# Kernel tuning notes

Measured on AMD Instinct MI355X. Metric: run time of the kernel, lower is better.

The kernel has to match this reference:

```python
import jax, jax.numpy as jnp
import numpy as np
from jax import lax

# db6 filters (pywt convention). rec_lo are the standard Daubechies-12 scaling coefs.
REC_LO = np.array([0.11154074335008017, 0.4946238903983854, 0.7511339080215775,
                   0.3152503517092432, -0.22626469396516913, -0.12976686756709563,
                   0.09750160558707936, 0.02752286553001629, -0.031582039318031156,
                   0.0005538422009938016, 0.004777257511010651, -0.00107730108499558])
L = 12
# qmf: rec_hi[n] = (-1)^n * rec_lo[L-1-n]
REC_HI = np.array([(-1.0)**n * REC_LO[L - 1 - n] for n in range(L)])
DEC_LO = REC_LO[::-1].copy()
DEC_HI = REC_HI[::-1].copy()
J = 8  # level1
DN = ('NCH', 'OIH', 'NCH')

def _afb(x):
    # one analysis level, symmetric padding (matches pytorch_wavelets afb1d).
    B, C, N = x.shape
    outsize = (N + L - 1) // 2
    p = 2 * (outsize - 1) - N + L
    xp = jnp.pad(x, ((0, 0), (0, 0), (p // 2, p - p // 2)), mode='symmetric')
    # torch conv1d correlates with reversed dec filters == rec filters
    k = jnp.stack([jnp.asarray(REC_LO, x.dtype), jnp.asarray(REC_HI, x.dtype)])[:, None, :]
    y = lax.conv_general_dilated(xp.reshape(B * C, 1, -1), k, (2,), 'VALID',
                                 dimension_numbers=DN)  # (B*C, 2, outsize)
    y = y.reshape(B, C, 2, outsize)
    return y[:, :, 0], y[:, :, 1]

def _sfb(lo, hi):
    # one synthesis level: conv_transpose1d(stride=2, padding=L-2) with rec filters
    # == dilate-by-2, pad 1 each side, correlate with flipped rec (= dec) filters.
    B, C, N = lo.shape
    def up(z, k):
        kk = jnp.asarray(k, z.dtype)[None, None, :]
        return lax.conv_general_dilated(z.reshape(B * C, 1, N), kk, (1,), [(1, 1)],
                                        lhs_dilation=(2,), dimension_numbers=DN).reshape(B, C, -1)
    return up(lo, DEC_LO) + up(hi, DEC_HI)  # length 2N - L + 2

def setup_inputs() -> dict:
    key = jax.random.key(0)
    k1, k2, k3 = jax.random.split(key, 3)
    Cin, Cout = 64, 64
    scale = 1.0 / (Cin * Cout)
    x = jax.random.normal(k1, (256, Cin, 1024), dtype=jnp.float32)
    weights1 = scale * jax.random.uniform(k2, (Cin, Cout, J + 6), dtype=jnp.float32)
    weights2 = scale * jax.random.uniform(k3, (Cin, Cout, J + 6), dtype=jnp.float32)
    return {'x': x, 'weights1': weights1, 'weights2': weights2}

def reference(x, weights1, weights2):
    # DWT decompose: yh[0] finest ... yh[-1] coarsest (pytorch_wavelets order)
    lo = x
    highs = []
    for _ in range(J):
        lo, hi = _afb(lo)
        highs.append(hi)
    # channel mix on coarsest approx and coarsest detail
    lo = jnp.einsum('bix,iox->box', lo, weights1)
    highs[-1] = jnp.einsum('bix,iox->box', highs[-1], weights2)
    # IDWT reconstruct, trimming odd-length mismatches like pytorch_wavelets
    y = lo
    for hi in highs[::-1]:
        if y.shape[-1] > hi.shape[-1]:
            y = y[..., :hi.shape[-1]]
        y = _sfb(y, hi)
    return y
```

## Files before the change

### kernel.cpp

```cpp
#include <hip/hip_runtime.h>

typedef float f2 __attribute__((ext_vector_type(2)));
typedef _Float16 half_t;
typedef _Float16 h4 __attribute__((ext_vector_type(4)));
typedef _Float16 h8 __attribute__((ext_vector_type(8)));

static constexpr float REC_LO[12] = {
  0.11154074335008017f, 0.4946238903983854f, 0.7511339080215775f, 0.3152503517092432f,
  -0.22626469396516913f, -0.12976686756709563f, 0.09750160558707936f, 0.02752286553001629f,
  -0.031582039318031156f, 0.0005538422009938016f, 0.004777257511010651f, -0.00107730108499558f };
static constexpr float REC_HI[12] = {
  -0.00107730108499558f, -0.004777257511010651f, 0.0005538422009938016f, 0.031582039318031156f,
  0.02752286553001629f, -0.09750160558707936f, -0.12976686756709563f, 0.22626469396516913f,
  0.3152503517092432f, -0.7511339080215775f, 0.4946238903983854f, -0.11154074335008017f };
static constexpr float DEC_LO[12] = {
  -0.00107730108499558f, 0.004777257511010651f, 0.0005538422009938016f, -0.031582039318031156f,
  0.02752286553001629f, 0.09750160558707936f, -0.12976686756709563f, -0.22626469396516913f,
  0.3152503517092432f, 0.7511339080215775f, 0.4946238903983854f, 0.11154074335008017f };
static constexpr float DEC_HI[12] = {
  -0.11154074335008017f, 0.4946238903983854f, -0.7511339080215775f, 0.3152503517092432f,
  0.22626469396516913f, -0.12976686756709563f, -0.09750160558707936f, 0.02752286553001629f,
  0.031582039318031156f, 0.0005538422009938016f, -0.004777257511010651f, -0.00107730108499558f };

#define NROWS 16384
#define WPB 4


__global__ __launch_bounds__(256) void afb_fused(const float* __restrict__ x,
                                                 half_t* __restrict__ ws) {
  __shared__ float sA[WPB][548];
  __shared__ float sB[WPB][296];
  constexpr int LENS[9] = {1024, 517, 264, 137, 74, 42, 26, 18, 14};
  constexpr int HSTR[8] = {520, 264, 144, 80, 48, 32, 24, 16};
  constexpr int HOFF[8] = {0, 520, 784, 928, 1008, 1056, 1088, 1112};
  const int wid = threadIdx.x >> 6;
  const int lane = threadIdx.x & 63;
  const int row = blockIdx.x * WPB + wid;
  float* bufA = sA[wid];
  float* bufB = sB[wid];
  const float* xrow = x + (size_t)row * 1024;
  half_t* hi0 = ws + (size_t)row * 520;

  {
    const int q = lane;
    const int base = (q == 0) ? 0 : 16 * q - 12;
    float xv[28];
#pragma unroll
    for (int r = 0; r < 7; ++r) {
      float4 v = *reinterpret_cast<const float4*>(xrow + base + 4 * r);
      xv[4 * r] = v.x; xv[4 * r + 1] = v.y; xv[4 * r + 2] = v.z; xv[4 * r + 3] = v.w;
    }
    float w[26];
    if (q == 0) {
#pragma unroll
      for (int e = 0; e < 26; ++e) w[e] = xv[e < 10 ? 9 - e : e - 10];
    } else {
#pragma unroll
      for (int e = 0; e < 26; ++e) w[e] = xv[2 + e];
    }
    f2 a[8];
#pragma unroll
    for (int d = 0; d < 8; ++d) a[d] = (f2){0.f, 0.f};
#pragma unroll
    for (int k = 0; k < 12; ++k) {
      f2 c = (f2){REC_LO[k], REC_HI[k]};
#pragma unroll
      for (int d = 0; d < 8; ++d) a[d] += w[2 * d + k] * c;
    }
#pragma unroll
    for (int d = 0; d < 4; ++d)
      *reinterpret_cast<f2*>(bufA + 14 + 8 * q + 2 * d) = (f2){a[2 * d].x, a[2 * d + 1].x};
    h8 hh;
#pragma unroll
    for (int d = 0; d < 8; ++d) hh[d] = (half_t)a[d].y;
    *reinterpret_cast<h8*>(hi0 + 8 * q) = hh;
  }
  if (lane < 5) {
    const int i0 = 1014 + 2 * lane;
    float acL = 0.f, acH = 0.f;
#pragma unroll
    for (int k = 0; k < 12; ++k) {
      int idx = i0 + k;
      idx = min(idx, 2047 - idx);
      float v = xrow[idx];
      acL += v * REC_LO[k];
      acH += v * REC_HI[k];
    }
    bufA[14 + 512 + lane] = acL;
    hi0[512 + lane] = (half_t)acH;
  }
  if (lane < 21) {
    int d, s;
    if (lane < 10) { d = 13 - lane; s = 14 + lane; }
    else { int k = lane - 10; d = 14 + 517 + k; s = 14 + 516 - k; }
    bufA[d] = bufA[s];
  }

  if (lane < 33) {
    const float* pp = bufA + 16 * lane + 4;
    float xv[28];
#pragma unroll
    for (int r = 0; r < 7; ++r) {
      float4 v = *reinterpret_cast<const float4*>(pp + 4 * r);
      xv[4 * r] = v.x; xv[4 * r + 1] = v.y; xv[4 * r + 2] = v.z; xv[4 * r + 3] = v.w;
    }
    f2 a[8];
#pragma unroll
    for (int d = 0; d < 8; ++d) a[d] = (f2){0.f, 0.f};
#pragma unroll
    for (int k = 0; k < 12; ++k) {
      f2 c = (f2){REC_LO[k], REC_HI[k]};
#pragma unroll
      for (int d = 0; d < 8; ++d) a[d] += xv[2 * d + k] * c;
    }
#pragma unroll
    for (int d = 0; d < 4; ++d)
      *reinterpret_cast<f2*>(bufB + 14 + 8 * lane + 2 * d) = (f2){a[2 * d].x, a[2 * d + 1].x};
    h8 hh;
#pragma unroll
    for (int d = 0; d < 8; ++d) hh[d] = (half_t)a[d].y;
    *reinterpret_cast<h8*>(ws + (size_t)NROWS * 520 + (size_t)row * 264 + 8 * lane) = hh;
  }
  if (lane < 21) {
    int d, s;
    if (lane < 10) { d = 13 - lane; s = 14 + lane; }
    else { int k = lane - 10; d = 14 + 264 + k; s = 14 + 263 - k; }
    bufB[d] = bufB[s];
  }

  __syncthreads();
  if (wid != 0) return;

  const int sub = lane >> 4, l16 = lane & 15;
  const int prow = blockIdx.x * WPB + sub;
  float* cur = sB[sub];
  float* dst = sA[sub];
  constexpr int NITS[8] = {0, 0, 3, 2, 1, 1, 1, 1};
#pragma unroll
  for (int j = 2; j < 8; ++j) {
    const int outN = LENS[j + 1];
    const int NCH = (outN + 3) / 4;
    half_t* hiRow = ws + (size_t)NROWS * HOFF[j] + (size_t)prow * HSTR[j];
#pragma unroll
    for (int it = 0; it < NITS[j]; ++it) {
      const int q = it * 16 + l16;
      if (q < NCH) {
        const float* pp = cur + 8 * q + 4;
        float xv[20];
#pragma unroll
        for (int r = 0; r < 5; ++r) {
          float4 v = *reinterpret_cast<const float4*>(pp + 4 * r);
          xv[4 * r] = v.x; xv[4 * r + 1] = v.y; xv[4 * r + 2] = v.z; xv[4 * r + 3] = v.w;
        }
        f2 a0 = {0.f, 0.f}, a1 = {0.f, 0.f}, a2 = {0.f, 0.f}, a3 = {0.f, 0.f};
#pragma unroll
        for (int k = 0; k < 12; ++k) {
          f2 c = (f2){REC_LO[k], REC_HI[k]};
          a0 += xv[k] * c; a1 += xv[2 + k] * c; a2 += xv[4 + k] * c; a3 += xv[6 + k] * c;
        }
        if (j < 7) {
          *reinterpret_cast<f2*>(dst + 14 + 4 * q) = (f2){a0.x, a1.x};
          *reinterpret_cast<f2*>(dst + 16 + 4 * q) = (f2){a2.x, a3.x};
        } else {
          h4 hl; hl[0] = (half_t)a0.x; hl[1] = (half_t)a1.x; hl[2] = (half_t)a2.x; hl[3] = (half_t)a3.x;
          *reinterpret_cast<h4*>(ws + (size_t)NROWS * 1128 + (size_t)prow * 16 + 4 * q) = hl;
        }
        h4 hh; hh[0] = (half_t)a0.y; hh[1] = (half_t)a1.y; hh[2] = (half_t)a2.y; hh[3] = (half_t)a3.y;
        *reinterpret_cast<h4*>(hiRow + 4 * q) = hh;
      }
    }
    if (j < 7) {
      if (l16 < 10) dst[13 - l16] = dst[14 + l16];
      if (l16 < 11) dst[14 + outN + l16] = dst[14 + outN - 1 - l16];
      float* t = cur; cur = dst; dst = t;
    }
  }
}

__global__ __launch_bounds__(256) void sfb_fused(const half_t* __restrict__ ws,
                                                 float* __restrict__ out) {
  __shared__ float sP[WPB][280];
  __shared__ float sQ[WPB][544];
  const int wid = threadIdx.x >> 6;
  const int lane = threadIdx.x & 63;

  if (wid == 0) {
    constexpr int LENSY[6] = {14, 18, 26, 42, 74, 137};
    constexpr int HSOFF[6] = {1144, 1088, 1056, 1008, 928, 784};
    constexpr int HSSTR[6] = {16, 24, 32, 48, 80, 144};
    constexpr int NITS[6] = {1, 1, 1, 1, 2, 3};
    const int sub = lane >> 4, l16 = lane & 15;
    const int prow = blockIdx.x * WPB + sub;
    float* cur = sP[sub];
    float* dst = sQ[sub];
    if (l16 < 2) {
      h8 v = *reinterpret_cast<const h8*>(ws + (size_t)NROWS * 1160 + (size_t)prow * 16 + 8 * l16);
      *reinterpret_cast<float4*>(cur + 8 * l16) =
          make_float4((float)v[0], (float)v[1], (float)v[2], (float)v[3]);
      *reinterpret_cast<float4*>(cur + 8 * l16 + 4) =
          make_float4((float)v[4], (float)v[5], (float)v[6], (float)v[7]);
    }
#pragma unroll
    for (int s = 0; s < 6; ++s) {
      const int N = LENSY[s];
      const int NP = N - 5;
      const int PCH = (NP + 3) / 4;
      const half_t* hsrc = ws + (size_t)NROWS * HSOFF[s] + (size_t)prow * HSSTR[s];
#pragma unroll
      for (int it = 0; it < NITS[s]; ++it) {
        const int q = it * 16 + l16;
        if (q < PCH) {
          const int m0 = 4 * q;
          float lv[9];
          {
            float4 a = *reinterpret_cast<const float4*>(cur + m0);
            float4 b = *reinterpret_cast<const float4*>(cur + m0 + 4);
            lv[0] = a.x; lv[1] = a.y; lv[2] = a.z; lv[3] = a.w;
            lv[4] = b.x; lv[5] = b.y; lv[6] = b.z; lv[7] = b.w;
            lv[8] = cur[m0 + 8];
          }
          float hv[9];
          {
            h4 h0 = *reinterpret_cast<const h4*>(hsrc + m0);
            h4 h1 = *reinterpret_cast<const h4*>(hsrc + m0 + 4);
            half_t h2 = hsrc[m0 + 8];
            hv[0] = (float)h0[0]; hv[1] = (float)h0[1]; hv[2] = (float)h0[2]; hv[3] = (float)h0[3];
            hv[4] = (float)h1[0]; hv[5] = (float)h1[1]; hv[6] = (float)h1[2]; hv[7] = (float)h1[3];
            hv[8] = (float)h2;
          }
          f2 a0 = {0.f, 0.f}, a1 = {0.f, 0.f}, a2 = {0.f, 0.f}, a3 = {0.f, 0.f};
#pragma unroll
          for (int t = 0; t < 6; ++t) {
            f2 dl = (f2){DEC_LO[2 * t + 1], DEC_LO[2 * t]};
            f2 dh = (f2){DEC_HI[2 * t + 1], DEC_HI[2 * t]};
            a0 += lv[t] * dl + hv[t] * dh;
            a1 += lv[1 + t] * dl + hv[1 + t] * dh;
            a2 += lv[2 + t] * dl + hv[2 + t] * dh;
            a3 += lv[3 + t] * dl + hv[3 + t] * dh;
          }
          *reinterpret_cast<float4*>(dst + 2 * m0)     = make_float4(a0.x, a0.y, a1.x, a1.y);
          *reinterpret_cast<float4*>(dst + 2 * m0 + 4) = make_float4(a2.x, a2.y, a3.x, a3.y);
        }
      }
      float* t = cur; cur = dst; dst = t;
    }
  }
  __syncthreads();

  const int row = blockIdx.x * WPB + wid;
  float* cur = sP[wid];
  float* dst = sQ[wid];
  {
    const half_t* hsrc = ws + (size_t)NROWS * 520 + (size_t)row * 264;
#pragma unroll
    for (int q0 = 0; q0 < 65; q0 += 64) {
      const int q = q0 + lane;
      if (q < 65) {
        const int m0 = 4 * q;
        float lv[9];
        {
          float4 a = *reinterpret_cast<const float4*>(cur + m0);
          float4 b = *reinterpret_cast<const float4*>(cur + m0 + 4);
          lv[0] = a.x; lv[1] = a.y; lv[2] = a.z; lv[3] = a.w;
          lv[4] = b.x; lv[5] = b.y; lv[6] = b.z; lv[7] = b.w;
          lv[8] = cur[m0 + 8];
        }
        float hv[9];
        {
          h4 h0 = *reinterpret_cast<const h4*>(hsrc + m0);
          h4 h1 = *reinterpret_cast<const h4*>(hsrc + m0 + 4);
          half_t h2 = hsrc[m0 + 8];
          hv[0] = (float)h0[0]; hv[1] = (float)h0[1]; hv[2] = (float)h0[2]; hv[3] = (float)h0[3];
          hv[4] = (float)h1[0]; hv[5] = (float)h1[1]; hv[6] = (float)h1[2]; hv[7] = (float)h1[3];
          hv[8] = (float)h2;
        }
        f2 a0 = {0.f, 0.f}, a1 = {0.f, 0.f}, a2 = {0.f, 0.f}, a3 = {0.f, 0.f};
#pragma unroll
        for (int t = 0; t < 6; ++t) {
          f2 dl = (f2){DEC_LO[2 * t + 1], DEC_LO[2 * t]};
          f2 dh = (f2){DEC_HI[2 * t + 1], DEC_HI[2 * t]};
          a0 += lv[t] * dl + hv[t] * dh;
          a1 += lv[1 + t] * dl + hv[1 + t] * dh;
          a2 += lv[2 + t] * dl + hv[2 + t] * dh;
          a3 += lv[3 + t] * dl + hv[3 + t] * dh;
        }
        *reinterpret_cast<float4*>(dst + 2 * m0)     = make_float4(a0.x, a0.y, a1.x, a1.y);
        *reinterpret_cast<float4*>(dst + 2 * m0 + 4) = make_float4(a2.x, a2.y, a3.x, a3.y);
      }
    }
  }
  {
    const half_t* hsrc = ws + (size_t)row * 520;
    float* orow = out + (size_t)row * 1024;
#pragma unroll
    for (int q0 = 0; q0 < 128; q0 += 64) {
      const int m0 = 4 * (q0 + lane);
      float lv[9];
      {
        float4 a = *reinterpret_cast<const float4*>(dst + m0);
        float4 b = *reinterpret_cast<const float4*>(dst + m0 + 4);
        lv[0] = a.x; lv[1] = a.y; lv[2] = a.z; lv[3] = a.w;
        lv[4] = b.x; lv[5] = b.y; lv[6] = b.z; lv[7] = b.w;
        lv[8] = dst[m0 + 8];
      }
      float hv[9];
      {
        h4 h0 = *reinterpret_cast<const h4*>(hsrc + m0);
        h4 h1 = *reinterpret_cast<const h4*>(hsrc + m0 + 4);
        half_t h2 = hsrc[m0 + 8];
        hv[0] = (float)h0[0]; hv[1] = (float)h0[1]; hv[2] = (float)h0[2]; hv[3] = (float)h0[3];
        hv[4] = (float)h1[0]; hv[5] = (float)h1[1]; hv[6] = (float)h1[2]; hv[7] = (float)h1[3];
        hv[8] = (float)h2;
      }
      f2 a0 = {0.f, 0.f}, a1 = {0.f, 0.f}, a2 = {0.f, 0.f}, a3 = {0.f, 0.f};
#pragma unroll
      for (int t = 0; t < 6; ++t) {
        f2 dl = (f2){DEC_LO[2 * t + 1], DEC_LO[2 * t]};
        f2 dh = (f2){DEC_HI[2 * t + 1], DEC_HI[2 * t]};
        a0 += lv[t] * dl + hv[t] * dh;
        a1 += lv[1 + t] * dl + hv[1 + t] * dh;
        a2 += lv[2 + t] * dl + hv[2 + t] * dh;
        a3 += lv[3 + t] * dl + hv[3 + t] * dh;
      }
      *reinterpret_cast<float4*>(orow + 2 * m0)     = make_float4(a0.x, a0.y, a1.x, a1.y);
      *reinterpret_cast<float4*>(orow + 2 * m0 + 4) = make_float4(a2.x, a2.y, a3.x, a3.y);
    }
  }
}

__global__ void mix_both(half_t* __restrict__ ws, const float* __restrict__ w1,
                         const float* __restrict__ w2) {
  __shared__ float s_in[2][896];
  const int which = blockIdx.x >> 7;
  const half_t* in = ws + (size_t)NROWS * (which ? 1112 : 1128);
  const float* w = which ? w2 : w1;
  half_t* out = ws + (size_t)NROWS * (which ? 1144 : 1160);
  int b0 = (blockIdx.x & 127) * 2;
  int t = threadIdx.x;
  int i = t / 14, xx = t % 14;
#pragma unroll
  for (int bb = 0; bb < 2; ++bb)
    s_in[bb][t] = (float)in[((size_t)(b0 + bb) * 64 + i) * 16 + xx];
  __syncthreads();
  float acc0 = 0.f, acc1 = 0.f;
#pragma unroll 8
  for (int k = 0; k < 64; ++k) {
    float wv = w[k * 896 + t];
    acc0 += s_in[0][k * 14 + xx] * wv;
    acc1 += s_in[1][k * 14 + xx] * wv;
  }
  out[((size_t)b0 * 64 + i) * 16 + xx] = (half_t)acc0;
  out[((size_t)(b0 + 1) * 64 + i) * 16 + xx] = (half_t)acc1;
}

extern "C" void kernel_launch(void* const* d_in, const int* in_sizes, int n_in,
                              void* d_out, int out_size, void* d_ws, size_t ws_size,
                              hipStream_t stream) {
  (void)in_sizes; (void)n_in; (void)out_size; (void)ws_size;
  const float* x  = (const float*)d_in[0];
  const float* w1 = (const float*)d_in[1];
  const float* w2 = (const float*)d_in[2];
  float* out = (float*)d_out;
  half_t* ws = (half_t*)d_ws;

  afb_fused<<<NROWS / WPB, 64 * WPB, 0, stream>>>(x, ws);
  mix_both<<<256, 896, 0, stream>>>(ws, w1, w2);
  sfb_fused<<<NROWS / WPB, 64 * WPB, 0, stream>>>(ws, out);
}
```

Before: 63.28 us.

## Fuse channel-mix einsum into synthesis kernel and drop separate mix launch

Removes the standalone mix_both kernel. Each synthesis block now computes the coarsest-level channel mix for its own rows directly from the workspace and weights into shared memory, then runs the first synthesis level from shared memory. This drops one kernel launch and the global round-trip of the mixed coefficients. The cost is that lanes 32–63 of warp 0 sit idle during the mix, and the first synthesis level waits on a 64-iteration reduction. It also flattens the 65-chunk level loop into one chunk per lane plus a 3-lane tail. The padding zero-fill for hmS uses a negative index, so it writes outside that array and leaves its tail uninitialised.

```diff
diff --git a/kernel.cpp b/kernel.cpp
--- a/kernel.cpp
+++ b/kernel.cpp
@@ -178,36 +178,84 @@
 }
 
 __global__ __launch_bounds__(256) void sfb_fused(const half_t* __restrict__ ws,
+                                                 const float* __restrict__ w1,
+                                                 const float* __restrict__ w2,
                                                  float* __restrict__ out) {
   __shared__ float sP[WPB][280];
   __shared__ float sQ[WPB][544];
+  __shared__ float loM[WPB][20];
+  __shared__ float hmS[WPB][20];
   const int wid = threadIdx.x >> 6;
   const int lane = threadIdx.x & 63;
 
   if (wid == 0) {
-    constexpr int LENSY[6] = {14, 18, 26, 42, 74, 137};
-    constexpr int HSOFF[6] = {1144, 1088, 1056, 1008, 928, 784};
-    constexpr int HSSTR[6] = {16, 24, 32, 48, 80, 144};
-    constexpr int NITS[6] = {1, 1, 1, 1, 2, 3};
+    const int row0 = blockIdx.x * WPB;
+    if (lane < 32) {
+      const int kind = lane >> 4;
+      const int c = (lane >> 2) & 3;
+      const int xg = lane & 3;
+      const int b = row0 >> 6;
+      const int cg = (row0 & 63) + c;
+      const half_t* inb = ws + (size_t)NROWS * (kind ? 1112 : 1128) + (size_t)(b * 64) * 16 + 4 * xg;
+      const float* wb = (kind ? w2 : w1) + cg * 14 + 4 * xg;
+      float a0 = 0.f, a1 = 0.f, a2 = 0.f, a3 = 0.f;
+#pragma unroll 8
+      for (int i = 0; i < 64; ++i) {
+        h4 iv = *reinterpret_cast<const h4*>(inb + (size_t)i * 16);
+        const float* wp = wb + (size_t)i * 896;
+        if (xg < 3) {
+          float4 wv = *reinterpret_cast<const float4*>(wp);
+          a0 += (float)iv[0] * wv.x; a1 += (float)iv[1] * wv.y;
+          a2 += (float)iv[2] * wv.z; a3 += (float)iv[3] * wv.w;
+        } else {
+          f2 wv = *reinterpret_cast<const f2*>(wp);
+          a0 += (float)iv[0] * wv.x; a1 += (float)iv[1] * wv.y;
+        }
+      }
+      float* o = (kind ? hmS[c] : loM[c]) + 4 * xg;
+      o[0] = a0; o[1] = a1; o[2] = a2; o[3] = a3;
+    } else {
+      int t = lane - 32;
+      if (t < 16) loM[t >> 2][16 + (t & 3)] = 0.f;
+      else { t -= 16; hmS[(t - 16) >> 2][16 + ((t - 16) & 3)] = 0.f; }
+    }
+
     const int sub = lane >> 4, l16 = lane & 15;
-    const int prow = blockIdx.x * WPB + sub;
-    float* cur = sP[sub];
+    const int prow = row0 + sub;
+    float* cur;
     float* dst = sQ[sub];
-    if (l16 < 2) {
-      h8 v = *reinterpret_cast<const h8*>(ws + (size_t)NROWS * 1160 + (size_t)prow * 16 + 8 * l16);
-      *reinterpret_cast<float4*>(cur + 8 * l16) =
-          make_float4((float)v[0], (float)v[1], (float)v[2], (float)v[3]);
-      *reinterpret_cast<float4*>(cur + 8 * l16 + 4) =
-          make_float4((float)v[4], (float)v[5], (float)v[6], (float)v[7]);
-    }
-#pragma unroll
-    for (int s = 0; s < 6; ++s) {
-      const int N = LENSY[s];
+    if (l16 < 3) {
+      const int m0 = 4 * l16;
+      float lv[9], hv[9];
+#pragma unroll
+      for (int e = 0; e < 9; ++e) { lv[e] = loM[sub][m0 + e]; hv[e] = hmS[sub][m0 + e]; }
+      f2 a0 = {0.f, 0.f}, a1 = {0.f, 0.f}, a2 = {0.f, 0.f}, a3 = {0.f, 0.f};
+#pragma unroll
+      for (int t = 0; t < 6; ++t) {
+        f2 dl = (f2){DEC_LO[2 * t + 1], DEC_LO[2 * t]};
+        f2 dh = (f2){DEC_HI[2 * t + 1], DEC_HI[2 * t]};
+        a0 += lv[t] * dl + hv[t] * dh;
+        a1 += lv[1 + t] * dl + hv[1 + t] * dh;
+        a2 += lv[2 + t] * dl + hv[2 + t] * dh;
+        a3 += lv[3 + t] * dl + hv[3 + t] * dh;
+      }
+      *reinterpret_cast<float4*>(dst + 2 * m0)     = make_float4(a0.x, a0.y, a1.x, a1.y);
+      *reinterpret_cast<float4*>(dst + 2 * m0 + 4) = make_float4(a2.x, a2.y, a3.x, a3.y);
+    }
+    cur = sQ[sub];
+    dst = sP[sub];
+    constexpr int LENSY2[5] = {18, 26, 42, 74, 137};
+    constexpr int HSOFF2[5] = {1088, 1056, 1008, 928, 784};
+    constexpr int HSSTR2[5] = {24, 32, 48, 80, 144};
+    constexpr int NITS2[5] = {1, 1, 1, 2, 3};
+#pragma unroll
+    for (int s = 0; s < 5; ++s) {
+      const int N = LENSY2[s];
       const int NP = N - 5;
       const int PCH = (NP + 3) / 4;
-      const half_t* hsrc = ws + (size_t)NROWS * HSOFF[s] + (size_t)prow * HSSTR[s];
-#pragma unroll
-      for (int it = 0; it < NITS[s]; ++it) {
+      const half_t* hsrc = ws + (size_t)NROWS * HSOFF2[s] + (size_t)prow * HSSTR2[s];
+#pragma unroll
+      for (int it = 0; it < NITS2[s]; ++it) {
         const int q = it * 16 + l16;
         if (q < PCH) {
           const int m0 = 4 * q;
@@ -252,41 +300,47 @@
   float* dst = sQ[wid];
   {
     const half_t* hsrc = ws + (size_t)NROWS * 520 + (size_t)row * 264;
-#pragma unroll
-    for (int q0 = 0; q0 < 65; q0 += 64) {
-      const int q = q0 + lane;
-      if (q < 65) {
-        const int m0 = 4 * q;
-        float lv[9];
-        {
-          float4 a = *reinterpret_cast<const float4*>(cur + m0);
-          float4 b = *reinterpret_cast<const float4*>(cur + m0 + 4);
-          lv[0] = a.x; lv[1] = a.y; lv[2] = a.z; lv[3] = a.w;
-          lv[4] = b.x; lv[5] = b.y; lv[6] = b.z; lv[7] = b.w;
-          lv[8] = cur[m0 + 8];
-        }
-        float hv[9];
-        {
-          h4 h0 = *reinterpret_cast<const h4*>(hsrc + m0);
-          h4 h1 = *reinterpret_cast<const h4*>(hsrc + m0 + 4);
-          half_t h2 = hsrc[m0 + 8];
-          hv[0] = (float)h0[0]; hv[1] = (float)h0[1]; hv[2] = (float)h0[2]; hv[3] = (float)h0[3];
-          hv[4] = (float)h1[0]; hv[5] = (float)h1[1]; hv[6] = (float)h1[2]; hv[7] = (float)h1[3];
-          hv[8] = (float)h2;
-        }
-        f2 a0 = {0.f, 0.f}, a1 = {0.f, 0.f}, a2 = {0.f, 0.f}, a3 = {0.f, 0.f};
-#pragma unroll
-        for (int t = 0; t < 6; ++t) {
-          f2 dl = (f2){DEC_LO[2 * t + 1], DEC_LO[2 * t]};
-          f2 dh = (f2){DEC_HI[2 * t + 1], DEC_HI[2 * t]};
-          a0 += lv[t] * dl + hv[t] * dh;
-          a1 += lv[1 + t] * dl + hv[1 + t] * dh;
-          a2 += lv[2 + t] * dl + hv[2 + t] * dh;
-          a3 += lv[3 + t] * dl + hv[3 + t] * dh;
-        }
-        *reinterpret_cast<float4*>(dst + 2 * m0)     = make_float4(a0.x, a0.y, a1.x, a1.y);
-        *reinterpret_cast<float4*>(dst + 2 * m0 + 4) = make_float4(a2.x, a2.y, a3.x, a3.y);
-      }
+    const int m0 = 4 * lane;
+    float lv[9];
+    {
+      float4 a = *reinterpret_cast<const float4*>(cur + m0);
+      float4 b = *reinterpret_cast<const float4*>(cur + m0 + 4);
+      lv[0] = a.x; lv[1] = a.y; lv[2] = a.z; lv[3] = a.w;
+      lv[4] = b.x; lv[5] = b.y; lv[6] = b.z; lv[7] = b.w;
+      lv[8] = cur[m0 + 8];
+    }
+    float hv[9];
+    {
+      h4 h0 = *reinterpret_cast<const h4*>(hsrc + m0);
+      h4 h1 = *reinterpret_cast<const h4*>(hsrc + m0 + 4);
+      half_t h2 = hsrc[m0 + 8];
+      hv[0] = (float)h0[0]; hv[1] = (float)h0[1]; hv[2] = (float)h0[2]; hv[3] = (float)h0[3];
+      hv[4] = (float)h1[0]; hv[5] = (float)h1[1]; hv[6] = (float)h1[2]; hv[7] = (float)h1[3];
+      hv[8] = (float)h2;
+    }
+    f2 a0 = {0.f, 0.f}, a1 = {0.f, 0.f}, a2 = {0.f, 0.f}, a3 = {0.f, 0.f};
+#pragma unroll
+    for (int t = 0; t < 6; ++t) {
+      f2 dl = (f2){DEC_LO[2 * t + 1], DEC_LO[2 * t]};
+      f2 dh = (f2){DEC_HI[2 * t + 1], DEC_HI[2 * t]};
+      a0 += lv[t] * dl + hv[t] * dh;
+      a1 += lv[1 + t] * dl + hv[1 + t] * dh;
+      a2 += lv[2 + t] * dl + hv[2 + t] * dh;
+      a3 += lv[3 + t] * dl + hv[3 + t] * dh;
+    }
+    *reinterpret_cast<float4*>(dst + 2 * m0)     = make_float4(a0.x, a0.y, a1.x, a1.y);
+    *reinterpret_cast<float4*>(dst + 2 * m0 + 4) = make_float4(a2.x, a2.y, a3.x, a3.y);
+    if (lane < 3) {
+      const int m = 256 + lane;
+      float aE = 0.f, aO = 0.f;
+#pragma unroll
+      for (int t = 0; t < 6; ++t) {
+        float lvv = cur[m + t];
+        float hvv = (float)hsrc[m + t];
+        aE += lvv * DEC_LO[2 * t + 1] + hvv * DEC_HI[2 * t + 1];
+        aO += lvv * DEC_LO[2 * t]     + hvv * DEC_HI[2 * t];
+      }
+      *reinterpret_cast<f2*>(dst + 2 * m) = (f2){aE, aO};
     }
   }
   {
@@ -328,31 +382,6 @@
   }
 }
 
-__global__ void mix_both(half_t* __restrict__ ws, const float* __restrict__ w1,
-                         const float* __restrict__ w2) {
-  __shared__ float s_in[2][896];
-  const int which = blockIdx.x >> 7;
-  const half_t* in = ws + (size_t)NROWS * (which ? 1112 : 1128);
-  const float* w = which ? w2 : w1;
-  half_t* out = ws + (size_t)NROWS * (which ? 1144 : 1160);
-  int b0 = (blockIdx.x & 127) * 2;
-  int t = threadIdx.x;
-  int i = t / 14, xx = t % 14;
-#pragma unroll
-  for (int bb = 0; bb < 2; ++bb)
-    s_in[bb][t] = (float)in[((size_t)(b0 + bb) * 64 + i) * 16 + xx];
-  __syncthreads();
-  float acc0 = 0.f, acc1 = 0.f;
-#pragma unroll 8
-  for (int k = 0; k < 64; ++k) {
-    float wv = w[k * 896 + t];
-    acc0 += s_in[0][k * 14 + xx] * wv;
-    acc1 += s_in[1][k * 14 + xx] * wv;
-  }
-  out[((size_t)b0 * 64 + i) * 16 + xx] = (half_t)acc0;
-  out[((size_t)(b0 + 1) * 64 + i) * 16 + xx] = (half_t)acc1;
-}
-
 extern "C" void kernel_launch(void* const* d_in, const int* in_sizes, int n_in,
                               void* d_out, int out_size, void* d_ws, size_t ws_size,
                               hipStream_t stream) {
@@ -364,6 +393,5 @@
   half_t* ws = (half_t*)d_ws;
 
   afb_fused<<<NROWS / WPB, 64 * WPB, 0, stream>>>(x, ws);
-  mix_both<<<256, 896, 0, stream>>>(ws, w1, w2);
-  sfb_fused<<<NROWS / WPB, 64 * WPB, 0, stream>>>(ws, out);
+  sfb_fused<<<NROWS / WPB, 64 * WPB, 0, stream>>>(ws, w1, w2, out);
 }
```

Result: slower. 128.2 us (+102.7%).
